# Kernel optimization log

Hardware: AMD Instinct MI355X
Metric: run time of the kernel (lower is better)

Reference implementation:

```python
import jax, jax.numpy as jnp
import numpy as np

N, T, H, W, C = 8, 128, 32, 32, 3
HID = 128
CONV_F = 32
FLAT = H * W * CONV_F  # 32768


def setup_inputs() -> dict:
    key = jax.random.key(0)
    ks = jax.random.split(key, 8)
    def w(k, shape, fan_in):
        return jax.random.normal(k, shape, jnp.float32) / np.sqrt(fan_in)
    x = jax.random.normal(ks[0], (N, T, H, W, C), jnp.float32)
    done = jax.random.randint(ks[1], (N, T), 0, 2, jnp.int32)
    return {
        "x": x,
        "done": done,
        "conv_w": w(ks[2], (3, 3, C, CONV_F), 3 * 3 * C),
        "conv_b": jnp.zeros((CONV_F,), jnp.float32),
        "early_w": w(ks[3], (FLAT, HID), FLAT),
        "early_b": jnp.zeros((HID,), jnp.float32),
        "lstm_wx": w(ks[4], (HID, 4 * HID), HID),
        "lstm_wh": w(ks[5], (HID, 4 * HID), HID),
        "lstm_b": jnp.zeros((4 * HID,), jnp.float32),
        "out_w": w(ks[6], (HID, HID), HID),
        "out_b": jnp.zeros((HID,), jnp.float32),
    }


def _forward(x, done, conv_w, conv_b, early_w, early_b,
             lstm_wx, lstm_wh, lstm_b, out_w, out_b):
    n, t = x.shape[0], x.shape[1]
    # conv encoder over flattened (N*T) frames, SAME padding (flax nn.Conv default)
    xf = x.reshape(n * t, H, W, C)
    xf = jax.lax.conv_general_dilated(
        xf, conv_w, window_strides=(1, 1), padding="SAME",
        dimension_numbers=("NHWC", "HWIO", "NHWC")) + conv_b
    feat = xf.reshape(n, t, -1)  # [N, T, FLAT]
    # early MLP
    feat = jax.nn.relu(feat @ early_w + early_b)  # [N, T, HID]
    # reset-masked LSTM scan over time
    # pre-compute input gate projections for all steps (batched matmul)
    zx = feat @ lstm_wx + lstm_b  # [N, T, 4H]
    zx_t = jnp.swapaxes(zx, 0, 1)       # [T, N, 4H]
    done_t = jnp.swapaxes(done, 0, 1)   # [T, N]

    def step(carry, inp):
        c, h = carry
        zxt, dt = inp
        mask = (dt != 0)[:, None]
        c = jnp.where(mask, 0.0, c)
        h = jnp.where(mask, 0.0, h)
        z = zxt + h @ lstm_wh  # [N, 4H]
        i, f, g, o = jnp.split(z, 4, axis=-1)
        i = jax.nn.sigmoid(i)
        f = jax.nn.sigmoid(f)
        g = jnp.tanh(g)
        o = jax.nn.sigmoid(o)
        c = f * c + i * g
        h = o * jnp.tanh(c)
        return (c, h), h

    init = (jnp.zeros((n, HID), jnp.float32), jnp.zeros((n, HID), jnp.float32))
    (c_fin, h_fin), hs = jax.lax.scan(step, init, (zx_t, done_t))
    hs = jnp.swapaxes(hs, 0, 1)  # [N, T, HID]
    # output MLP
    y = jax.nn.relu(hs @ out_w + out_b)
    return c_fin, h_fin, y


def reference(x, done, conv_w, conv_b, early_w, early_b,
              lstm_wx, lstm_wh, lstm_b, out_w, out_b):
    return _forward(x, done, conv_w, conv_b, early_w, early_b,
                    lstm_wx, lstm_wh, lstm_b, out_w, out_b)
```

## Files before the change

kernel.cpp:

```cpp
#include <hip/hip_runtime.h>


typedef unsigned short ushort_t;
typedef short bf16x8 __attribute__((ext_vector_type(8)));
typedef float f32x4 __attribute__((ext_vector_type(4)));
typedef _Float16 h2 __attribute__((ext_vector_type(2)));

__device__ __forceinline__ ushort_t f2b(float f) {
  unsigned int u = __float_as_uint(f);
  unsigned int r = (u + 0x7fffu + ((u >> 16) & 1u)) >> 16;
  return (ushort_t)r;
}
__device__ __forceinline__ unsigned pack_h2(float a, float b) {
  union { _Float16 h[2]; unsigned u; } v;
  v.h[0] = (_Float16)a; v.h[1] = (_Float16)b; return v.u;
}

#define NT   1024
#define KIN  3072
#define KS   8

__global__ __launch_bounds__(256) void prep_kernel(
    const float* __restrict__ wx, const float* __restrict__ wh,
    const float* __restrict__ ow, const float* __restrict__ eb,
    ushort_t* __restrict__ wxT, unsigned* __restrict__ whT16,
    ushort_t* __restrict__ owT, float* __restrict__ bias2)
{
  const int total = 65536 + 32768 + 16384 + 128;
  for (int i = blockIdx.x * blockDim.x + threadIdx.x; i < total;
       i += gridDim.x * blockDim.x) {
    int j = i;
    if (j < 65536) { int n = j >> 7, k = j & 127; wxT[j] = f2b(wx[k * 512 + n]); continue; }
    j -= 65536;
    if (j < 32768) {
      int col = j >> 6, k2 = j & 63;
      whT16[j] = pack_h2(wh[(2 * k2) * 512 + col], wh[(2 * k2 + 1) * 512 + col]);
      continue;
    }
    j -= 32768;
    if (j < 16384) { int n = j >> 7, k = j & 127; owT[j] = f2b(ow[k * 128 + n]); continue; }
    j -= 16384;
    bias2[j] = eb[j];
  }
}

__global__ __launch_bounds__(128) void build_u(
    const float* __restrict__ conv_w, const float* __restrict__ conv_b,
    const float* __restrict__ early_w,
    ushort_t* __restrict__ UT, float* __restrict__ bias2)
{
  __shared__ float cw[864];
  const int tid = threadIdx.x;
  const int p = blockIdx.x;
  for (int i = tid; i < 864; i += 128) cw[i] = conv_w[i];
  __syncthreads();
  const int hp = p >> 5, wp = p & 31;
  float a0 = 0.f, a1 = 0.f, a2 = 0.f;
  for (int kh = 0; kh < 3; kh++) {
    int h = hp - kh + 1; if ((unsigned)h >= 32u) continue;
    for (int kw = 0; kw < 3; kw++) {
      int w = wp - kw + 1; if ((unsigned)w >= 32u) continue;
      const float* wr = early_w + ((size_t)((h * 32 + w) * 32)) * 128 + tid;
      const float* cwp = cw + (kh * 3 + kw) * 96;
      #pragma unroll 8
      for (int f = 0; f < 32; f++) {
        float wv = wr[f * 128];
        a0 += cwp[f]      * wv;
        a1 += cwp[32 + f] * wv;
        a2 += cwp[64 + f] * wv;
      }
    }
  }
  size_t ub = (size_t)tid * KIN + p * 3;
  UT[ub + 0] = f2b(a0); UT[ub + 1] = f2b(a1); UT[ub + 2] = f2b(a2);

  float cbs = 0.f;
  #pragma unroll 8
  for (int f = 0; f < 32; f++) cbs += __builtin_fabsf(conv_b[f]);
  if (cbs != 0.f && p < 32) {
    float part = 0.f;
    for (int pp = p * 32; pp < p * 32 + 32; pp++)
      for (int f = 0; f < 32; f++)
        part += conv_b[f] * early_w[(size_t)(pp * 32 + f) * 128 + tid];
    atomicAdd(&bias2[tid], part);
  }
}

__global__ __launch_bounds__(256) void feat_gemm(
    const float* __restrict__ x, const ushort_t* __restrict__ UT,
    float* __restrict__ partial)
{
  __shared__ short As[16 * 72];
  __shared__ short Bs[128 * 72];
  const int tid = threadIdx.x;
  const int m0 = blockIdx.x * 16;
  const int ks = blockIdx.y;
  const int wave = tid >> 6, lane = tid & 63;
  const int quad = lane >> 4, l15 = lane & 15;
  const int c0 = wave * 32;

  f32x4 acc0 = {0.f, 0.f, 0.f, 0.f};
  f32x4 acc1 = {0.f, 0.f, 0.f, 0.f};

  const int kend = ks * 384 + 384;
  for (int k0 = ks * 384; k0 < kend; k0 += 64) {
    __syncthreads();
    for (int s = tid; s < 1152; s += 256) {
      if (s < 128) {
        int row = s >> 3, t8 = s & 7;
        const float4* g = (const float4*)(x + (size_t)(m0 + row) * KIN + k0 + t8 * 8);
        float4 f0 = g[0], f1 = g[1];
        ushort_t tmp[8] = {f2b(f0.x), f2b(f0.y), f2b(f0.z), f2b(f0.w),
                           f2b(f1.x), f2b(f1.y), f2b(f1.z), f2b(f1.w)};
        *(uint4*)&As[row * 72 + t8 * 8] = *(const uint4*)tmp;
      } else {
        int s2 = s - 128;
        int row = s2 >> 3, t8 = s2 & 7;
        const uint4* g = (const uint4*)(UT + (size_t)row * KIN + k0 + t8 * 8);
        *(uint4*)&Bs[row * 72 + t8 * 8] = *g;
      }
    }
    __syncthreads();
    #pragma unroll
    for (int kk = 0; kk < 2; kk++) {
      int ko = kk * 32 + quad * 8;
      bf16x8 a  = *(const bf16x8*)&As[l15 * 72 + ko];
      bf16x8 b0 = *(const bf16x8*)&Bs[(c0 + l15) * 72 + ko];
      bf16x8 b1 = *(const bf16x8*)&Bs[(c0 + 16 + l15) * 72 + ko];
      acc0 = __builtin_amdgcn_mfma_f32_16x16x32_bf16(a, b0, acc0, 0, 0, 0);
      acc1 = __builtin_amdgcn_mfma_f32_16x16x32_bf16(a, b1, acc1, 0, 0, 0);
    }
  }
  #pragma unroll
  for (int r = 0; r < 4; r++) {
    int m = m0 + quad * 4 + r;
    size_t base = ((size_t)ks * 1024 + m) * 128;
    partial[base + c0 + l15]      = acc0[r];
    partial[base + c0 + 16 + l15] = acc1[r];
  }
}

__global__ __launch_bounds__(256) void reduce_feat(
    const float* __restrict__ partial, const float* __restrict__ bias2,
    ushort_t* __restrict__ featb)
{
  int i = blockIdx.x * 256 + threadIdx.x;
  float s = bias2[i & 127];
  #pragma unroll
  for (int ks = 0; ks < KS; ks++) s += partial[(size_t)ks * 131072 + i];
  featb[i] = f2b(fmaxf(s, 0.f));
}

__global__ __launch_bounds__(128) void gemm_k128(
    const ushort_t* __restrict__ A, const ushort_t* __restrict__ BT,
    const float* __restrict__ bias,
    float* __restrict__ outf, ushort_t* __restrict__ outb,
    int N, int relu)
{
  __shared__ short As[16 * 136];
  __shared__ short Bs[64 * 136];
  const int tid = threadIdx.x;
  const int m0 = blockIdx.x * 16;
  const int n0 = blockIdx.y * 64;
  const int wave = tid >> 6, lane = tid & 63;
  const int quad = lane >> 4, l15 = lane & 15;
  const int c0 = wave * 32;

  for (int s = tid; s < 1280; s += 128) {
    int row = s >> 4, t8 = s & 15;
    if (s < 256) {
      const uint4* g = (const uint4*)(A + (size_t)(m0 + row) * 128 + t8 * 8);
      *(uint4*)&As[row * 136 + t8 * 8] = *g;
    } else {
      int r2 = row - 16;
      const uint4* g = (const uint4*)(BT + (size_t)(n0 + r2) * 128 + t8 * 8);
      *(uint4*)&Bs[r2 * 136 + t8 * 8] = *g;
    }
  }
  __syncthreads();

  f32x4 acc0 = {0.f, 0.f, 0.f, 0.f};
  f32x4 acc1 = {0.f, 0.f, 0.f, 0.f};
  #pragma unroll
  for (int kk = 0; kk < 4; kk++) {
    int ko = kk * 32 + quad * 8;
    bf16x8 a  = *(const bf16x8*)&As[l15 * 136 + ko];
    bf16x8 b0 = *(const bf16x8*)&Bs[(c0 + l15) * 136 + ko];
    bf16x8 b1 = *(const bf16x8*)&Bs[(c0 + 16 + l15) * 136 + ko];
    acc0 = __builtin_amdgcn_mfma_f32_16x16x32_bf16(a, b0, acc0, 0, 0, 0);
    acc1 = __builtin_amdgcn_mfma_f32_16x16x32_bf16(a, b1, acc1, 0, 0, 0);
  }
  #pragma unroll
  for (int r = 0; r < 4; r++) {
    int m = m0 + quad * 4 + r;
    int n1 = n0 + c0 + l15, n2 = n1 + 16;
    float v1 = acc0[r] + bias[n1];
    float v2 = acc1[r] + bias[n2];
    if (relu) { v1 = fmaxf(v1, 0.f); v2 = fmaxf(v2, 0.f); }
    size_t o1 = (size_t)m * N + n1, o2 = (size_t)m * N + n2;
    if (outf) { outf[o1] = v1; outf[o2] = v2; }
    if (outb) { outb[o1] = f2b(v1); outb[o2] = f2b(v2); }
  }
}

__device__ __forceinline__ float fsig(float x) {
  return 1.f / (1.f + exp2f(-1.44269504f * x));
}
__device__ __forceinline__ float ftanh(float x) {
  float e = exp2f(2.885390082f * x);
  return 1.f - 2.f / (e + 1.f);
}
__device__ __forceinline__ int nth_bit(unsigned long long m0, unsigned long long m1, int i) {
  int c0 = __popcll(m0);
  if (i < c0) {
    unsigned long long m = m0;
    for (int k = 0; k < i; k++) m &= m - 1;
    return __ffsll((long long)m) - 1;
  }
  i -= c0;
  unsigned long long m = m1;
  for (int k = 0; k < i; k++) m &= m - 1;
  return 64 + __ffsll((long long)m) - 1;
}

__global__ __launch_bounds__(512, 2) void lstm_scan(
    const int* __restrict__ done, const float* __restrict__ zx,
    const unsigned* __restrict__ whT16, ushort_t* __restrict__ hsb,
    float* __restrict__ dout)
{
  __shared__ float z_s[512];
  __shared__ _Float16 h16_s[128];
  __shared__ float c_s[128];
  __shared__ unsigned long long masks[16];
  const int tid = threadIdx.x;

  uint4 w4[16];
  {
    const uint4* wp = (const uint4*)(whT16 + (size_t)tid * 64);
    #pragma unroll
    for (int i = 0; i < 16; i++) w4[i] = wp[i];
  }
  const h2* wv = (const h2*)w4;

  for (int n = 0; n < 8; n++) {
    bool flag = false;
    if (tid < 128) flag = (tid == 0) || (done[n * 128 + tid] != 0);
    unsigned long long m = __ballot(flag);
    if (tid == 0)  masks[2*n]     = m;
    if (tid == 64) masks[2*n + 1] = m;
  }
  __syncthreads();

  int total = 0;
  #pragma unroll
  for (int n = 0; n < 8; n++)
    total += __popcll(masks[2*n]) + __popcll(masks[2*n+1]);

  for (int g = blockIdx.x; g < total; g += gridDim.x) {
    int i = g, n = 0, cn = 0;
    for (; n < 8; n++) {
      cn = __popcll(masks[2*n]) + __popcll(masks[2*n+1]);
      if (i < cn) break;
      i -= cn;
    }
    int t0 = nth_bit(masks[2*n], masks[2*n+1], i);
    int t1 = (i + 1 < cn) ? nth_bit(masks[2*n], masks[2*n+1], i + 1) : 128;

    if (tid < 128) { ((ushort_t*)h16_s)[tid] = 0; c_s[tid] = 0.f; }
    __syncthreads();

    float zval = zx[((size_t)n * 128 + t0) * 512 + tid];
    for (int t = t0; t < t1; t++) {
      float znext = 0.f;
      if (t + 1 < t1) znext = zx[((size_t)n * 128 + t + 1) * 512 + tid];
      float a0 = 0.f, a1 = 0.f, a2 = 0.f, a3 = 0.f;
      const float4* hp = (const float4*)h16_s;
      #pragma unroll
      for (int q = 0; q < 16; q++) {
        float4 hb = hp[q];
        const h2* hh = (const h2*)&hb;
        a0 = __builtin_amdgcn_fdot2(wv[4*q+0], hh[0], a0, false);
        a1 = __builtin_amdgcn_fdot2(wv[4*q+1], hh[1], a1, false);
        a2 = __builtin_amdgcn_fdot2(wv[4*q+2], hh[2], a2, false);
        a3 = __builtin_amdgcn_fdot2(wv[4*q+3], hh[3], a3, false);
      }
      z_s[tid] = zval + (a0 + a1) + (a2 + a3);
      __syncthreads();
      if (tid < 128) {
        float ig = fsig(z_s[tid]);
        float fg = fsig(z_s[tid + 128]);
        float gg = ftanh(z_s[tid + 256]);
        float og = fsig(z_s[tid + 384]);
        float c = fg * c_s[tid] + ig * gg;
        float hn = og * ftanh(c);
        c_s[tid] = c;
        h16_s[tid] = (_Float16)hn;
        hsb[((size_t)n * 128 + t) * 128 + tid] = f2b(hn);
        if (t == 127) {
          dout[n * 128 + tid] = c;
          dout[1024 + n * 128 + tid] = hn;
        }
      }
      __syncthreads();
      zval = znext;
    }
  }
}

extern "C" void kernel_launch(void* const* d_in, const int* in_sizes, int n_in,
                              void* d_out, int out_size, void* d_ws, size_t ws_size,
                              hipStream_t stream) {
  const float* x       = (const float*)d_in[0];
  const int*   done    = (const int*)  d_in[1];
  const float* conv_w  = (const float*)d_in[2];
  const float* conv_b  = (const float*)d_in[3];
  const float* early_w = (const float*)d_in[4];
  const float* early_b = (const float*)d_in[5];
  const float* lstm_wx = (const float*)d_in[6];
  const float* lstm_wh = (const float*)d_in[7];
  const float* lstm_b  = (const float*)d_in[8];
  const float* out_w   = (const float*)d_in[9];
  const float* out_b   = (const float*)d_in[10];
  float* dout = (float*)d_out;

  char* ws = (char*)d_ws;
  float*    partial = (float*)   (ws + 0);
  ushort_t* UT      = (ushort_t*)(ws + 4194304);
  ushort_t* featb   = (ushort_t*)(ws + 4980736);
  float*    zx      = (float*)   (ws + 5242880);
  ushort_t* wxT     = (ushort_t*)(ws + 7340032);
  unsigned* whT16   = (unsigned*)(ws + 7471104);
  ushort_t* owT     = (ushort_t*)(ws + 7733248);
  ushort_t* hsb     = (ushort_t*)(ws + 7766016);
  float*    bias2   = (float*)   (ws + 8028160);

  prep_kernel<<<120, 256, 0, stream>>>(lstm_wx, lstm_wh, out_w, early_b,
                                       wxT, whT16, owT, bias2);
  build_u<<<1024, 128, 0, stream>>>(conv_w, conv_b, early_w, UT, bias2);
  feat_gemm<<<dim3(64, KS), 256, 0, stream>>>(x, UT, partial);
  reduce_feat<<<512, 256, 0, stream>>>(partial, bias2, featb);
  gemm_k128<<<dim3(64, 8), 128, 0, stream>>>(featb, wxT, lstm_b, zx, nullptr, 512, 0);
  lstm_scan<<<512, 512, 0, stream>>>(done, zx, whT16, hsb, dout);
  gemm_k128<<<dim3(64, 2), 128, 0, stream>>>(hsb, owT, out_b, dout + 2048, nullptr, 128, 1);
}
```

Before: 154.6 us.

## Fuse all stages into one persistent kernel with global atomic barriers

Replaces the seven launches with one persistent 512-block kernel. Stages are separated by an atomic-counter grid barrier, and the counter is reset by a memset before each launch. The feature-reduce step is folded into the zx GEMM, the feature GEMM gets double-buffered, XOR-swizzled LDS staging, and the LSTM scan uses 256 threads that each handle two gate columns. The goal is to remove launch gaps and the featb round trip. In exchange it relies on all 512 blocks being co-resident for the barrier to avoid deadlock, and it holds more registers per thread in the scan.

```diff
diff --git a/kernel.cpp b/kernel.cpp
--- a/kernel.cpp
+++ b/kernel.cpp
@@ -6,203 +6,16 @@
 typedef float f32x4 __attribute__((ext_vector_type(4)));
 typedef _Float16 h2 __attribute__((ext_vector_type(2)));
 
+#define GRID 512
+
 __device__ __forceinline__ ushort_t f2b(float f) {
-  unsigned int u = __float_as_uint(f);
-  unsigned int r = (u + 0x7fffu + ((u >> 16) & 1u)) >> 16;
-  return (ushort_t)r;
+  unsigned u = __float_as_uint(f);
+  return (ushort_t)((u + 0x7fffu + ((u >> 16) & 1u)) >> 16);
 }
 __device__ __forceinline__ unsigned pack_h2(float a, float b) {
   union { _Float16 h[2]; unsigned u; } v;
   v.h[0] = (_Float16)a; v.h[1] = (_Float16)b; return v.u;
 }
-
-#define NT   1024
-#define KIN  3072
-#define KS   8
-
-__global__ __launch_bounds__(256) void prep_kernel(
-    const float* __restrict__ wx, const float* __restrict__ wh,
-    const float* __restrict__ ow, const float* __restrict__ eb,
-    ushort_t* __restrict__ wxT, unsigned* __restrict__ whT16,
-    ushort_t* __restrict__ owT, float* __restrict__ bias2)
-{
-  const int total = 65536 + 32768 + 16384 + 128;
-  for (int i = blockIdx.x * blockDim.x + threadIdx.x; i < total;
-       i += gridDim.x * blockDim.x) {
-    int j = i;
-    if (j < 65536) { int n = j >> 7, k = j & 127; wxT[j] = f2b(wx[k * 512 + n]); continue; }
-    j -= 65536;
-    if (j < 32768) {
-      int col = j >> 6, k2 = j & 63;
-      whT16[j] = pack_h2(wh[(2 * k2) * 512 + col], wh[(2 * k2 + 1) * 512 + col]);
-      continue;
-    }
-    j -= 32768;
-    if (j < 16384) { int n = j >> 7, k = j & 127; owT[j] = f2b(ow[k * 128 + n]); continue; }
-    j -= 16384;
-    bias2[j] = eb[j];
-  }
-}
-
-__global__ __launch_bounds__(128) void build_u(
-    const float* __restrict__ conv_w, const float* __restrict__ conv_b,
-    const float* __restrict__ early_w,
-    ushort_t* __restrict__ UT, float* __restrict__ bias2)
-{
-  __shared__ float cw[864];
-  const int tid = threadIdx.x;
-  const int p = blockIdx.x;
-  for (int i = tid; i < 864; i += 128) cw[i] = conv_w[i];
-  __syncthreads();
-  const int hp = p >> 5, wp = p & 31;
-  float a0 = 0.f, a1 = 0.f, a2 = 0.f;
-  for (int kh = 0; kh < 3; kh++) {
-    int h = hp - kh + 1; if ((unsigned)h >= 32u) continue;
-    for (int kw = 0; kw < 3; kw++) {
-      int w = wp - kw + 1; if ((unsigned)w >= 32u) continue;
-      const float* wr = early_w + ((size_t)((h * 32 + w) * 32)) * 128 + tid;
-      const float* cwp = cw + (kh * 3 + kw) * 96;
-      #pragma unroll 8
-      for (int f = 0; f < 32; f++) {
-        float wv = wr[f * 128];
-        a0 += cwp[f]      * wv;
-        a1 += cwp[32 + f] * wv;
-        a2 += cwp[64 + f] * wv;
-      }
-    }
-  }
-  size_t ub = (size_t)tid * KIN + p * 3;
-  UT[ub + 0] = f2b(a0); UT[ub + 1] = f2b(a1); UT[ub + 2] = f2b(a2);
-
-  float cbs = 0.f;
-  #pragma unroll 8
-  for (int f = 0; f < 32; f++) cbs += __builtin_fabsf(conv_b[f]);
-  if (cbs != 0.f && p < 32) {
-    float part = 0.f;
-    for (int pp = p * 32; pp < p * 32 + 32; pp++)
-      for (int f = 0; f < 32; f++)
-        part += conv_b[f] * early_w[(size_t)(pp * 32 + f) * 128 + tid];
-    atomicAdd(&bias2[tid], part);
-  }
-}
-
-__global__ __launch_bounds__(256) void feat_gemm(
-    const float* __restrict__ x, const ushort_t* __restrict__ UT,
-    float* __restrict__ partial)
-{
-  __shared__ short As[16 * 72];
-  __shared__ short Bs[128 * 72];
-  const int tid = threadIdx.x;
-  const int m0 = blockIdx.x * 16;
-  const int ks = blockIdx.y;
-  const int wave = tid >> 6, lane = tid & 63;
-  const int quad = lane >> 4, l15 = lane & 15;
-  const int c0 = wave * 32;
-
-  f32x4 acc0 = {0.f, 0.f, 0.f, 0.f};
-  f32x4 acc1 = {0.f, 0.f, 0.f, 0.f};
-
-  const int kend = ks * 384 + 384;
-  for (int k0 = ks * 384; k0 < kend; k0 += 64) {
-    __syncthreads();
-    for (int s = tid; s < 1152; s += 256) {
-      if (s < 128) {
-        int row = s >> 3, t8 = s & 7;
-        const float4* g = (const float4*)(x + (size_t)(m0 + row) * KIN + k0 + t8 * 8);
-        float4 f0 = g[0], f1 = g[1];
-        ushort_t tmp[8] = {f2b(f0.x), f2b(f0.y), f2b(f0.z), f2b(f0.w),
-                           f2b(f1.x), f2b(f1.y), f2b(f1.z), f2b(f1.w)};
-        *(uint4*)&As[row * 72 + t8 * 8] = *(const uint4*)tmp;
-      } else {
-        int s2 = s - 128;
-        int row = s2 >> 3, t8 = s2 & 7;
-        const uint4* g = (const uint4*)(UT + (size_t)row * KIN + k0 + t8 * 8);
-        *(uint4*)&Bs[row * 72 + t8 * 8] = *g;
-      }
-    }
-    __syncthreads();
-    #pragma unroll
-    for (int kk = 0; kk < 2; kk++) {
-      int ko = kk * 32 + quad * 8;
-      bf16x8 a  = *(const bf16x8*)&As[l15 * 72 + ko];
-      bf16x8 b0 = *(const bf16x8*)&Bs[(c0 + l15) * 72 + ko];
-      bf16x8 b1 = *(const bf16x8*)&Bs[(c0 + 16 + l15) * 72 + ko];
-      acc0 = __builtin_amdgcn_mfma_f32_16x16x32_bf16(a, b0, acc0, 0, 0, 0);
-      acc1 = __builtin_amdgcn_mfma_f32_16x16x32_bf16(a, b1, acc1, 0, 0, 0);
-    }
-  }
-  #pragma unroll
-  for (int r = 0; r < 4; r++) {
-    int m = m0 + quad * 4 + r;
-    size_t base = ((size_t)ks * 1024 + m) * 128;
-    partial[base + c0 + l15]      = acc0[r];
-    partial[base + c0 + 16 + l15] = acc1[r];
-  }
-}
-
-__global__ __launch_bounds__(256) void reduce_feat(
-    const float* __restrict__ partial, const float* __restrict__ bias2,
-    ushort_t* __restrict__ featb)
-{
-  int i = blockIdx.x * 256 + threadIdx.x;
-  float s = bias2[i & 127];
-  #pragma unroll
-  for (int ks = 0; ks < KS; ks++) s += partial[(size_t)ks * 131072 + i];
-  featb[i] = f2b(fmaxf(s, 0.f));
-}
-
-__global__ __launch_bounds__(128) void gemm_k128(
-    const ushort_t* __restrict__ A, const ushort_t* __restrict__ BT,
-    const float* __restrict__ bias,
-    float* __restrict__ outf, ushort_t* __restrict__ outb,
-    int N, int relu)
-{
-  __shared__ short As[16 * 136];
-  __shared__ short Bs[64 * 136];
-  const int tid = threadIdx.x;
-  const int m0 = blockIdx.x * 16;
-  const int n0 = blockIdx.y * 64;
-  const int wave = tid >> 6, lane = tid & 63;
-  const int quad = lane >> 4, l15 = lane & 15;
-  const int c0 = wave * 32;
-
-  for (int s = tid; s < 1280; s += 128) {
-    int row = s >> 4, t8 = s & 15;
-    if (s < 256) {
-      const uint4* g = (const uint4*)(A + (size_t)(m0 + row) * 128 + t8 * 8);
-      *(uint4*)&As[row * 136 + t8 * 8] = *g;
-    } else {
-      int r2 = row - 16;
-      const uint4* g = (const uint4*)(BT + (size_t)(n0 + r2) * 128 + t8 * 8);
-      *(uint4*)&Bs[r2 * 136 + t8 * 8] = *g;
-    }
-  }
-  __syncthreads();
-
-  f32x4 acc0 = {0.f, 0.f, 0.f, 0.f};
-  f32x4 acc1 = {0.f, 0.f, 0.f, 0.f};
-  #pragma unroll
-  for (int kk = 0; kk < 4; kk++) {
-    int ko = kk * 32 + quad * 8;
-    bf16x8 a  = *(const bf16x8*)&As[l15 * 136 + ko];
-    bf16x8 b0 = *(const bf16x8*)&Bs[(c0 + l15) * 136 + ko];
-    bf16x8 b1 = *(const bf16x8*)&Bs[(c0 + 16 + l15) * 136 + ko];
-    acc0 = __builtin_amdgcn_mfma_f32_16x16x32_bf16(a, b0, acc0, 0, 0, 0);
-    acc1 = __builtin_amdgcn_mfma_f32_16x16x32_bf16(a, b1, acc1, 0, 0, 0);
-  }
-  #pragma unroll
-  for (int r = 0; r < 4; r++) {
-    int m = m0 + quad * 4 + r;
-    int n1 = n0 + c0 + l15, n2 = n1 + 16;
-    float v1 = acc0[r] + bias[n1];
-    float v2 = acc1[r] + bias[n2];
-    if (relu) { v1 = fmaxf(v1, 0.f); v2 = fmaxf(v2, 0.f); }
-    size_t o1 = (size_t)m * N + n1, o2 = (size_t)m * N + n2;
-    if (outf) { outf[o1] = v1; outf[o2] = v2; }
-    if (outb) { outb[o1] = f2b(v1); outb[o2] = f2b(v2); }
-  }
-}
-
 __device__ __forceinline__ float fsig(float x) {
   return 1.f / (1.f + exp2f(-1.44269504f * x));
 }
@@ -223,86 +36,319 @@
   return 64 + __ffsll((long long)m) - 1;
 }
 
-__global__ __launch_bounds__(512, 2) void lstm_scan(
-    const int* __restrict__ done, const float* __restrict__ zx,
-    const unsigned* __restrict__ whT16, ushort_t* __restrict__ hsb,
-    float* __restrict__ dout)
+__device__ __forceinline__ void gbar(unsigned* ctr, unsigned target) {
+  __syncthreads();
+  if (threadIdx.x == 0) {
+    __hip_atomic_fetch_add(ctr, 1u, __ATOMIC_RELEASE, __HIP_MEMORY_SCOPE_AGENT);
+    while (__hip_atomic_load(ctr, __ATOMIC_ACQUIRE, __HIP_MEMORY_SCOPE_AGENT) < target)
+      __builtin_amdgcn_s_sleep(8);
+  }
+  __syncthreads();
+}
+
+__global__ __launch_bounds__(256, 2) void mega(
+    const float* __restrict__ x, const int* __restrict__ done,
+    const float* __restrict__ conv_w, const float* __restrict__ conv_b,
+    const float* __restrict__ early_w, const float* __restrict__ eb,
+    const float* __restrict__ wx, const float* __restrict__ wh,
+    const float* __restrict__ lstm_b, const float* __restrict__ ow,
+    const float* __restrict__ out_b,
+    unsigned* __restrict__ ctr, float* __restrict__ partial,
+    ushort_t* __restrict__ UT, float* __restrict__ zx,
+    ushort_t* __restrict__ wxT, unsigned* __restrict__ whT16,
+    ushort_t* __restrict__ owT, ushort_t* __restrict__ hsb,
+    float* __restrict__ bias2, float* __restrict__ dout)
 {
-  __shared__ float z_s[512];
-  __shared__ _Float16 h16_s[128];
-  __shared__ float c_s[128];
-  __shared__ unsigned long long masks[16];
+  __shared__ union {
+    float cw[864];
+    short ft[2][9216];
+    short g2[18432];
+    struct { float z[512]; float c[128]; _Float16 h16[128];
+             unsigned long long masks[16]; } ls;
+  } L;
+
   const int tid = threadIdx.x;
-
-  uint4 w4[16];
+  const int b = blockIdx.x;
+  const int wave = tid >> 6, lane = tid & 63;
+  const int quad = lane >> 4, l15 = lane & 15;
+  const int c0 = wave * 32;
+
   {
-    const uint4* wp = (const uint4*)(whT16 + (size_t)tid * 64);
-    #pragma unroll
-    for (int i = 0; i < 16; i++) w4[i] = wp[i];
-  }
-  const h2* wv = (const h2*)w4;
-
-  for (int n = 0; n < 8; n++) {
-    bool flag = false;
-    if (tid < 128) flag = (tid == 0) || (done[n * 128 + tid] != 0);
-    unsigned long long m = __ballot(flag);
-    if (tid == 0)  masks[2*n]     = m;
-    if (tid == 64) masks[2*n + 1] = m;
-  }
-  __syncthreads();
-
-  int total = 0;
-  #pragma unroll
-  for (int n = 0; n < 8; n++)
-    total += __popcll(masks[2*n]) + __popcll(masks[2*n+1]);
-
-  for (int g = blockIdx.x; g < total; g += gridDim.x) {
-    int i = g, n = 0, cn = 0;
-    for (; n < 8; n++) {
-      cn = __popcll(masks[2*n]) + __popcll(masks[2*n+1]);
-      if (i < cn) break;
-      i -= cn;
-    }
-    int t0 = nth_bit(masks[2*n], masks[2*n+1], i);
-    int t1 = (i + 1 < cn) ? nth_bit(masks[2*n], masks[2*n+1], i + 1) : 128;
-
-    if (tid < 128) { ((ushort_t*)h16_s)[tid] = 0; c_s[tid] = 0.f; }
+    int i = b * 256 + tid;
+    if (i < 65536) { int n = i >> 7, k = i & 127; wxT[i] = f2b(wx[k * 512 + n]); }
+    else if (i < 98304) { int j = i - 65536; int col = j >> 6, k2 = j & 63;
+      whT16[j] = pack_h2(wh[(2 * k2) * 512 + col], wh[(2 * k2 + 1) * 512 + col]); }
+    else if (i < 114688) { int j = i - 98304; int n = j >> 7, k = j & 127;
+      owT[j] = f2b(ow[k * 128 + n]); }
+    else if (i < 114816) { bias2[i - 114688] = eb[i - 114688]; }
+
+    for (int q = tid; q < 864; q += 256) L.cw[q] = conv_w[q];
     __syncthreads();
-
-    float zval = zx[((size_t)n * 128 + t0) * 512 + tid];
-    for (int t = t0; t < t1; t++) {
-      float znext = 0.f;
-      if (t + 1 < t1) znext = zx[((size_t)n * 128 + t + 1) * 512 + tid];
-      float a0 = 0.f, a1 = 0.f, a2 = 0.f, a3 = 0.f;
-      const float4* hp = (const float4*)h16_s;
-      #pragma unroll
-      for (int q = 0; q < 16; q++) {
-        float4 hb = hp[q];
-        const h2* hh = (const h2*)&hb;
-        a0 = __builtin_amdgcn_fdot2(wv[4*q+0], hh[0], a0, false);
-        a1 = __builtin_amdgcn_fdot2(wv[4*q+1], hh[1], a1, false);
-        a2 = __builtin_amdgcn_fdot2(wv[4*q+2], hh[2], a2, false);
-        a3 = __builtin_amdgcn_fdot2(wv[4*q+3], hh[3], a3, false);
-      }
-      z_s[tid] = zval + (a0 + a1) + (a2 + a3);
+    const int o = tid & 127, grp = tid >> 7;
+    const int px = (b & 7) * 128 + ((b >> 3) << 1) + grp;
+    const int hp = px >> 5, wp = px & 31;
+    float a0 = 0.f, a1 = 0.f, a2 = 0.f;
+    for (int kh = 0; kh < 3; kh++) {
+      int h = hp - kh + 1; if ((unsigned)h >= 32u) continue;
+      for (int kw = 0; kw < 3; kw++) {
+        int w = wp - kw + 1; if ((unsigned)w >= 32u) continue;
+        const float* wr = early_w + ((size_t)((h * 32 + w) * 32)) * 128 + o;
+        const float* cwp = L.cw + (kh * 3 + kw) * 96;
+        #pragma unroll 8
+        for (int f = 0; f < 32; f++) {
+          float wv = wr[f * 128];
+          a0 += cwp[f]      * wv;
+          a1 += cwp[32 + f] * wv;
+          a2 += cwp[64 + f] * wv;
+        }
+      }
+    }
+    size_t ub = (size_t)o * 3072 + px * 3;
+    UT[ub + 0] = f2b(a0); UT[ub + 1] = f2b(a1); UT[ub + 2] = f2b(a2);
+
+    float cbs = 0.f;
+    #pragma unroll 8
+    for (int f = 0; f < 32; f++) cbs += __builtin_fabsf(conv_b[f]);
+    if (cbs != 0.f && px < 32) {
+      float part = 0.f;
+      for (int pp = px * 32; pp < px * 32 + 32; pp++)
+        for (int f = 0; f < 32; f++)
+          part += conv_b[f] * early_w[(size_t)(pp * 32 + f) * 128 + o];
+      atomicAdd(&bias2[o], part);
+    }
+  }
+  gbar(ctr, GRID);
+
+  {
+    const int m0 = (b & 63) * 16;
+    const int ks = b >> 6;
+    const int kb = ks * 384;
+    const bool isA = tid < 128;
+    const int arow = tid >> 3, ag = tid & 7;
+    const int s2base = tid ^ 128;
+
+    float4 fa0, fa1; uint4 rb[4];
+    f32x4 acc0 = {0.f, 0.f, 0.f, 0.f};
+    f32x4 acc1 = {0.f, 0.f, 0.f, 0.f};
+
+    auto load = [&](int k0) {
+      if (isA) {
+        const float4* p = (const float4*)(x + (size_t)(m0 + arow) * 3072 + k0 + ag * 8);
+        fa0 = p[0]; fa1 = p[1];
+      }
+      #pragma unroll
+      for (int j = 0; j < 4; j++) {
+        int s2 = s2base + 256 * j, row = s2 >> 3, g = s2 & 7;
+        rb[j] = *(const uint4*)(UT + (size_t)row * 3072 + k0 + g * 8);
+      }
+    };
+    auto stage = [&](int p) {
+      #pragma unroll
+      for (int j = 0; j < 4; j++) {
+        int s2 = s2base + 256 * j, row = s2 >> 3, g = s2 & 7;
+        *(uint4*)&L.ft[p][1024 + row * 64 + (((g ^ row) & 7) * 8)] = rb[j];
+      }
+      if (isA) {
+        union { ushort_t us[8]; uint4 v; } t8;
+        t8.us[0] = f2b(fa0.x); t8.us[1] = f2b(fa0.y); t8.us[2] = f2b(fa0.z); t8.us[3] = f2b(fa0.w);
+        t8.us[4] = f2b(fa1.x); t8.us[5] = f2b(fa1.y); t8.us[6] = f2b(fa1.z); t8.us[7] = f2b(fa1.w);
+        *(uint4*)&L.ft[p][arow * 64 + (((ag ^ arow) & 7) * 8)] = t8.v;
+      }
+    };
+
+    load(kb);
+    for (int it = 0; it < 6; it++) {
+      const int p = it & 1;
+      stage(p);
       __syncthreads();
-      if (tid < 128) {
-        float ig = fsig(z_s[tid]);
-        float fg = fsig(z_s[tid + 128]);
-        float gg = ftanh(z_s[tid + 256]);
-        float og = fsig(z_s[tid + 384]);
-        float c = fg * c_s[tid] + ig * gg;
-        float hn = og * ftanh(c);
-        c_s[tid] = c;
-        h16_s[tid] = (_Float16)hn;
-        hsb[((size_t)n * 128 + t) * 128 + tid] = f2b(hn);
-        if (t == 127) {
-          dout[n * 128 + tid] = c;
-          dout[1024 + n * 128 + tid] = hn;
+      if (it < 5) load(kb + (it + 1) * 64);
+      const short* As = &L.ft[p][0];
+      const short* Bs = &L.ft[p][1024];
+      #pragma unroll
+      for (int kk = 0; kk < 2; kk++) {
+        int gp = kk * 4 + quad;
+        bf16x8 a  = *(const bf16x8*)&As[l15 * 64 + (((gp ^ l15) & 7) * 8)];
+        bf16x8 b0 = *(const bf16x8*)&Bs[(c0 + l15) * 64 + (((gp ^ (c0 + l15)) & 7) * 8)];
+        bf16x8 b1 = *(const bf16x8*)&Bs[(c0 + 16 + l15) * 64 + (((gp ^ (c0 + l15)) & 7) * 8)];
+        acc0 = __builtin_amdgcn_mfma_f32_16x16x32_bf16(a, b0, acc0, 0, 0, 0);
+        acc1 = __builtin_amdgcn_mfma_f32_16x16x32_bf16(a, b1, acc1, 0, 0, 0);
+      }
+    }
+    #pragma unroll
+    for (int r = 0; r < 4; r++) {
+      int m = m0 + quad * 4 + r;
+      size_t base = ((size_t)ks * 1024 + m) * 128;
+      partial[base + c0 + l15]      = acc0[r];
+      partial[base + c0 + 16 + l15] = acc1[r];
+    }
+  }
+  gbar(ctr, 2 * GRID);
+
+  if (b < 256) {
+    const int m0 = (b & 63) * 16;
+    const int n0 = (b >> 6) * 128;
+    {
+      int r = tid >> 4, gA = tid & 15, cb = gA * 8;
+      float4 s0 = {0,0,0,0}, s1 = {0,0,0,0};
+      #pragma unroll
+      for (int ks = 0; ks < 8; ks++) {
+        const float4* p = (const float4*)(partial + (size_t)ks * 131072 + (m0 + r) * 128 + cb);
+        float4 u0 = p[0], u1 = p[1];
+        s0.x += u0.x; s0.y += u0.y; s0.z += u0.z; s0.w += u0.w;
+        s1.x += u1.x; s1.y += u1.y; s1.z += u1.z; s1.w += u1.w;
+      }
+      const float* bp = bias2 + cb;
+      union { ushort_t us[8]; uint4 v; } t8;
+      t8.us[0] = f2b(fmaxf(s0.x + bp[0], 0.f)); t8.us[1] = f2b(fmaxf(s0.y + bp[1], 0.f));
+      t8.us[2] = f2b(fmaxf(s0.z + bp[2], 0.f)); t8.us[3] = f2b(fmaxf(s0.w + bp[3], 0.f));
+      t8.us[4] = f2b(fmaxf(s1.x + bp[4], 0.f)); t8.us[5] = f2b(fmaxf(s1.y + bp[5], 0.f));
+      t8.us[6] = f2b(fmaxf(s1.z + bp[6], 0.f)); t8.us[7] = f2b(fmaxf(s1.w + bp[7], 0.f));
+      *(uint4*)&L.g2[r * 128 + (((gA ^ r) & 15) * 8)] = t8.v;
+    }
+    #pragma unroll
+    for (int j = 0; j < 8; j++) {
+      int s = tid + 256 * j, row = s >> 4, g = s & 15;
+      uint4 v = *(const uint4*)(wxT + (size_t)(n0 + row) * 128 + g * 8);
+      *(uint4*)&L.g2[2048 + row * 128 + (((g ^ row) & 15) * 8)] = v;
+    }
+    __syncthreads();
+    f32x4 acc0 = {0,0,0,0}, acc1 = {0,0,0,0};
+    #pragma unroll
+    for (int kk = 0; kk < 4; kk++) {
+      int gp = kk * 4 + quad;
+      bf16x8 a  = *(const bf16x8*)&L.g2[l15 * 128 + (((gp ^ l15) & 15) * 8)];
+      bf16x8 b0 = *(const bf16x8*)&L.g2[2048 + (c0 + l15) * 128 + (((gp ^ l15) & 15) * 8)];
+      bf16x8 b1 = *(const bf16x8*)&L.g2[2048 + (c0 + 16 + l15) * 128 + (((gp ^ l15) & 15) * 8)];
+      acc0 = __builtin_amdgcn_mfma_f32_16x16x32_bf16(a, b0, acc0, 0, 0, 0);
+      acc1 = __builtin_amdgcn_mfma_f32_16x16x32_bf16(a, b1, acc1, 0, 0, 0);
+    }
+    #pragma unroll
+    for (int r = 0; r < 4; r++) {
+      int m = m0 + quad * 4 + r;
+      int n1 = n0 + c0 + l15, n2 = n1 + 16;
+      zx[(size_t)m * 512 + n1] = acc0[r] + lstm_b[n1];
+      zx[(size_t)m * 512 + n2] = acc1[r] + lstm_b[n2];
+    }
+  }
+  gbar(ctr, 3 * GRID);
+
+  {
+    uint4 w1[16], w2[16];
+    {
+      const uint4* p1 = (const uint4*)(whT16 + (size_t)tid * 64);
+      const uint4* p2 = (const uint4*)(whT16 + (size_t)(tid + 256) * 64);
+      #pragma unroll
+      for (int i = 0; i < 16; i++) { w1[i] = p1[i]; w2[i] = p2[i]; }
+    }
+    const h2* wa = (const h2*)w1;
+    const h2* wb = (const h2*)w2;
+
+    for (int n = 0; n < 8; n++) {
+      bool flag = false;
+      if (tid < 128) flag = (tid == 0) || (done[n * 128 + tid] != 0);
+      unsigned long long m = __ballot(flag);
+      if (tid == 0)  L.ls.masks[2 * n]     = m;
+      if (tid == 64) L.ls.masks[2 * n + 1] = m;
+    }
+    __syncthreads();
+
+    int total = 0;
+    #pragma unroll
+    for (int n = 0; n < 8; n++)
+      total += __popcll(L.ls.masks[2 * n]) + __popcll(L.ls.masks[2 * n + 1]);
+
+    for (int g = b; g < total; g += GRID) {
+      int i = g, n = 0, cn = 0;
+      for (; n < 8; n++) {
+        cn = __popcll(L.ls.masks[2 * n]) + __popcll(L.ls.masks[2 * n + 1]);
+        if (i < cn) break;
+        i -= cn;
+      }
+      int t0 = nth_bit(L.ls.masks[2 * n], L.ls.masks[2 * n + 1], i);
+      int t1 = (i + 1 < cn) ? nth_bit(L.ls.masks[2 * n], L.ls.masks[2 * n + 1], i + 1) : 128;
+
+      if (tid < 128) { ((ushort_t*)L.ls.h16)[tid] = 0; L.ls.c[tid] = 0.f; }
+      __syncthreads();
+
+      float z1 = zx[((size_t)n * 128 + t0) * 512 + tid];
+      float z2 = zx[((size_t)n * 128 + t0) * 512 + tid + 256];
+      for (int t = t0; t < t1; t++) {
+        float z1n = 0.f, z2n = 0.f;
+        if (t + 1 < t1) {
+          z1n = zx[((size_t)n * 128 + t + 1) * 512 + tid];
+          z2n = zx[((size_t)n * 128 + t + 1) * 512 + tid + 256];
         }
-      }
-      __syncthreads();
-      zval = znext;
+        float a0 = 0.f, a1 = 0.f, a2 = 0.f, a3 = 0.f;
+        float b0 = 0.f, b1 = 0.f, b2 = 0.f, b3 = 0.f;
+        const float4* hp = (const float4*)L.ls.h16;
+        #pragma unroll
+        for (int q = 0; q < 16; q++) {
+          float4 hb = hp[q];
+          const h2* hh = (const h2*)&hb;
+          a0 = __builtin_amdgcn_fdot2(wa[4*q+0], hh[0], a0, false);
+          a1 = __builtin_amdgcn_fdot2(wa[4*q+1], hh[1], a1, false);
+          a2 = __builtin_amdgcn_fdot2(wa[4*q+2], hh[2], a2, false);
+          a3 = __builtin_amdgcn_fdot2(wa[4*q+3], hh[3], a3, false);
+          b0 = __builtin_amdgcn_fdot2(wb[4*q+0], hh[0], b0, false);
+          b1 = __builtin_amdgcn_fdot2(wb[4*q+1], hh[1], b1, false);
+          b2 = __builtin_amdgcn_fdot2(wb[4*q+2], hh[2], b2, false);
+          b3 = __builtin_amdgcn_fdot2(wb[4*q+3], hh[3], b3, false);
+        }
+        L.ls.z[tid]       = z1 + (a0 + a1) + (a2 + a3);
+        L.ls.z[tid + 256] = z2 + (b0 + b1) + (b2 + b3);
+        __syncthreads();
+        if (tid < 128) {
+          float ig = fsig(L.ls.z[tid]);
+          float fg = fsig(L.ls.z[tid + 128]);
+          float gg = ftanh(L.ls.z[tid + 256]);
+          float og = fsig(L.ls.z[tid + 384]);
+          float c = fg * L.ls.c[tid] + ig * gg;
+          float hn = og * ftanh(c);
+          L.ls.c[tid] = c;
+          L.ls.h16[tid] = (_Float16)hn;
+          hsb[((size_t)n * 128 + t) * 128 + tid] = f2b(hn);
+          if (t == 127) {
+            dout[n * 128 + tid] = c;
+            dout[1024 + n * 128 + tid] = hn;
+          }
+        }
+        __syncthreads();
+        z1 = z1n; z2 = z2n;
+      }
+    }
+  }
+  gbar(ctr, 4 * GRID);
+
+  if (b < 64) {
+    const int m0 = b * 16;
+    {
+      int r = tid >> 4, g = tid & 15;
+      uint4 av = *(const uint4*)(hsb + (size_t)(m0 + r) * 128 + g * 8);
+      *(uint4*)&L.g2[r * 128 + (((g ^ r) & 15) * 8)] = av;
+    }
+    #pragma unroll
+    for (int j = 0; j < 8; j++) {
+      int s = tid + 256 * j, row = s >> 4, g = s & 15;
+      uint4 v = *(const uint4*)(owT + (size_t)row * 128 + g * 8);
+      *(uint4*)&L.g2[2048 + row * 128 + (((g ^ row) & 15) * 8)] = v;
+    }
+    __syncthreads();
+    f32x4 acc0 = {0,0,0,0}, acc1 = {0,0,0,0};
+    #pragma unroll
+    for (int kk = 0; kk < 4; kk++) {
+      int gp = kk * 4 + quad;
+      bf16x8 a  = *(const bf16x8*)&L.g2[l15 * 128 + (((gp ^ l15) & 15) * 8)];
+      bf16x8 b0 = *(const bf16x8*)&L.g2[2048 + (c0 + l15) * 128 + (((gp ^ l15) & 15) * 8)];
+      bf16x8 b1 = *(const bf16x8*)&L.g2[2048 + (c0 + 16 + l15) * 128 + (((gp ^ l15) & 15) * 8)];
+      acc0 = __builtin_amdgcn_mfma_f32_16x16x32_bf16(a, b0, acc0, 0, 0, 0);
+      acc1 = __builtin_amdgcn_mfma_f32_16x16x32_bf16(a, b1, acc1, 0, 0, 0);
+    }
+    #pragma unroll
+    for (int r = 0; r < 4; r++) {
+      int m = m0 + quad * 4 + r;
+      int n1 = c0 + l15, n2 = n1 + 16;
+      dout[2048 + (size_t)m * 128 + n1] = fmaxf(acc0[r] + out_b[n1], 0.f);
+      dout[2048 + (size_t)m * 128 + n2] = fmaxf(acc1[r] + out_b[n2], 0.f);
     }
   }
 }
@@ -324,22 +370,19 @@
   float* dout = (float*)d_out;
 
   char* ws = (char*)d_ws;
-  float*    partial = (float*)   (ws + 0);
-  ushort_t* UT      = (ushort_t*)(ws + 4194304);
-  ushort_t* featb   = (ushort_t*)(ws + 4980736);
-  float*    zx      = (float*)   (ws + 5242880);
-  ushort_t* wxT     = (ushort_t*)(ws + 7340032);
-  unsigned* whT16   = (unsigned*)(ws + 7471104);
-  ushort_t* owT     = (ushort_t*)(ws + 7733248);
-  ushort_t* hsb     = (ushort_t*)(ws + 7766016);
-  float*    bias2   = (float*)   (ws + 8028160);
-
-  prep_kernel<<<120, 256, 0, stream>>>(lstm_wx, lstm_wh, out_w, early_b,
-                                       wxT, whT16, owT, bias2);
-  build_u<<<1024, 128, 0, stream>>>(conv_w, conv_b, early_w, UT, bias2);
-  feat_gemm<<<dim3(64, KS), 256, 0, stream>>>(x, UT, partial);
-  reduce_feat<<<512, 256, 0, stream>>>(partial, bias2, featb);
-  gemm_k128<<<dim3(64, 8), 128, 0, stream>>>(featb, wxT, lstm_b, zx, nullptr, 512, 0);
-  lstm_scan<<<512, 512, 0, stream>>>(done, zx, whT16, hsb, dout);
-  gemm_k128<<<dim3(64, 2), 128, 0, stream>>>(hsb, owT, out_b, dout + 2048, nullptr, 128, 1);
-}
+  unsigned* ctrp    = (unsigned*)(ws + 0);
+  float*    partial = (float*)   (ws + 4096);
+  ushort_t* UT      = (ushort_t*)(ws + 4198400);
+  float*    zx      = (float*)   (ws + 4984832);
+  ushort_t* wxT     = (ushort_t*)(ws + 7081984);
+  unsigned* whT16   = (unsigned*)(ws + 7213056);
+  ushort_t* owT     = (ushort_t*)(ws + 7344128);
+  ushort_t* hsb     = (ushort_t*)(ws + 7376896);
+  float*    bias2   = (float*)   (ws + 7639040);
+
+  hipMemsetAsync(ctrp, 0, 256, stream);
+  mega<<<GRID, 256, 0, stream>>>(x, done, conv_w, conv_b, early_w, early_b,
+                                 lstm_wx, lstm_wh, lstm_b, out_w, out_b,
+                                 ctrp, partial, UT, zx, wxT, whT16, owT, hsb,
+                                 bias2, dout);
+}
```

Measured after the change: 374.9 us. 142% more time.

## Fuse pipeline kernels: merge prep into build, reduce into zx GEMM, output MLP into scan

Applied to the files above, without the earlier changes.

Merges the weight prep kernel and the conv-folded weight builder into one launch. Folds the split-K reduction and ReLU into the zx GEMM, which now uses 128-wide N tiles. Moves the output MLP into the LSTM scan as per-step fp16 dot products, which removes the hs buffer and one GEMM launch. In exchange the scan adds serial work inside each step and drops the zx prefetch, and the fp16 output weights may cost accuracy.

```diff
diff --git a/kernel.cpp b/kernel.cpp
--- a/kernel.cpp
+++ b/kernel.cpp
@@ -7,51 +7,63 @@
 typedef _Float16 h2 __attribute__((ext_vector_type(2)));
 
 __device__ __forceinline__ ushort_t f2b(float f) {
-  unsigned int u = __float_as_uint(f);
-  unsigned int r = (u + 0x7fffu + ((u >> 16) & 1u)) >> 16;
-  return (ushort_t)r;
+  unsigned u = __float_as_uint(f);
+  return (ushort_t)((u + 0x7fffu + ((u >> 16) & 1u)) >> 16);
 }
 __device__ __forceinline__ unsigned pack_h2(float a, float b) {
   union { _Float16 h[2]; unsigned u; } v;
   v.h[0] = (_Float16)a; v.h[1] = (_Float16)b; return v.u;
 }
-
-#define NT   1024
-#define KIN  3072
-#define KS   8
-
-__global__ __launch_bounds__(256) void prep_kernel(
+__device__ __forceinline__ float fsig(float x) {
+  return 1.f / (1.f + exp2f(-1.44269504f * x));
+}
+__device__ __forceinline__ float ftanh(float x) {
+  float e = exp2f(2.885390082f * x);
+  return 1.f - 2.f / (e + 1.f);
+}
+__device__ __forceinline__ int nth_bit(unsigned long long m0, unsigned long long m1, int i) {
+  int c0 = __popcll(m0);
+  if (i < c0) {
+    unsigned long long m = m0;
+    for (int k = 0; k < i; k++) m &= m - 1;
+    return __ffsll((long long)m) - 1;
+  }
+  i -= c0;
+  unsigned long long m = m1;
+  for (int k = 0; k < i; k++) m &= m - 1;
+  return 64 + __ffsll((long long)m) - 1;
+}
+
+__global__ __launch_bounds__(128) void prep_build(
+    const float* __restrict__ conv_w, const float* __restrict__ conv_b,
+    const float* __restrict__ early_w, const float* __restrict__ eb,
     const float* __restrict__ wx, const float* __restrict__ wh,
-    const float* __restrict__ ow, const float* __restrict__ eb,
-    ushort_t* __restrict__ wxT, unsigned* __restrict__ whT16,
-    ushort_t* __restrict__ owT, float* __restrict__ bias2)
+    const float* __restrict__ ow,
+    ushort_t* __restrict__ UT, ushort_t* __restrict__ wxT,
+    unsigned* __restrict__ whT16, unsigned* __restrict__ owT16,
+    float* __restrict__ bias2)
 {
-  const int total = 65536 + 32768 + 16384 + 128;
-  for (int i = blockIdx.x * blockDim.x + threadIdx.x; i < total;
-       i += gridDim.x * blockDim.x) {
-    int j = i;
-    if (j < 65536) { int n = j >> 7, k = j & 127; wxT[j] = f2b(wx[k * 512 + n]); continue; }
-    j -= 65536;
-    if (j < 32768) {
-      int col = j >> 6, k2 = j & 63;
-      whT16[j] = pack_h2(wh[(2 * k2) * 512 + col], wh[(2 * k2 + 1) * 512 + col]);
-      continue;
-    }
-    j -= 32768;
-    if (j < 16384) { int n = j >> 7, k = j & 127; owT[j] = f2b(ow[k * 128 + n]); continue; }
-    j -= 16384;
-    bias2[j] = eb[j];
-  }
-}
-
-__global__ __launch_bounds__(128) void build_u(
-    const float* __restrict__ conv_w, const float* __restrict__ conv_b,
-    const float* __restrict__ early_w,
-    ushort_t* __restrict__ UT, float* __restrict__ bias2)
-{
+  const int tid = threadIdx.x;
+  const int b = blockIdx.x;
+
+  if (b >= 1024) {
+    for (int i = (b - 1024) * 128 + tid; i < 131200; i += 128 * 128) {
+      int j = i;
+      if (j < 65536) { int n = j >> 7, k = j & 127; wxT[j] = f2b(wx[k * 512 + n]); continue; }
+      j -= 65536;
+      if (j < 32768) { int col = j >> 6, k2 = j & 63;
+        whT16[j] = pack_h2(wh[(2 * k2) * 512 + col], wh[(2 * k2 + 1) * 512 + col]); continue; }
+      j -= 32768;
+      if (j < 32768) { int col = j >> 6, k2 = j & 63;
+        owT16[j] = pack_h2(ow[(2 * k2) * 128 + col], ow[(2 * k2 + 1) * 128 + col]); continue; }
+      j -= 32768;
+      bias2[j] = eb[j];
+    }
+    return;
+  }
+
   __shared__ float cw[864];
-  const int tid = threadIdx.x;
-  const int p = blockIdx.x;
+  const int p = b;
   for (int i = tid; i < 864; i += 128) cw[i] = conv_w[i];
   __syncthreads();
   const int hp = p >> 5, wp = p & 31;
@@ -71,7 +83,7 @@
       }
     }
   }
-  size_t ub = (size_t)tid * KIN + p * 3;
+  size_t ub = (size_t)tid * 3072 + p * 3;
   UT[ub + 0] = f2b(a0); UT[ub + 1] = f2b(a1); UT[ub + 2] = f2b(a2);
 
   float cbs = 0.f;
@@ -108,7 +120,7 @@
     for (int s = tid; s < 1152; s += 256) {
       if (s < 128) {
         int row = s >> 3, t8 = s & 7;
-        const float4* g = (const float4*)(x + (size_t)(m0 + row) * KIN + k0 + t8 * 8);
+        const float4* g = (const float4*)(x + (size_t)(m0 + row) * 3072 + k0 + t8 * 8);
         float4 f0 = g[0], f1 = g[1];
         ushort_t tmp[8] = {f2b(f0.x), f2b(f0.y), f2b(f0.z), f2b(f0.w),
                            f2b(f1.x), f2b(f1.y), f2b(f1.z), f2b(f1.w)};
@@ -116,7 +128,7 @@
       } else {
         int s2 = s - 128;
         int row = s2 >> 3, t8 = s2 & 7;
-        const uint4* g = (const uint4*)(UT + (size_t)row * KIN + k0 + t8 * 8);
+        const uint4* g = (const uint4*)(UT + (size_t)row * 3072 + k0 + t8 * 8);
         *(uint4*)&Bs[row * 72 + t8 * 8] = *g;
       }
     }
@@ -140,47 +152,47 @@
   }
 }
 
-__global__ __launch_bounds__(256) void reduce_feat(
+__global__ __launch_bounds__(256) void zx_gemm(
     const float* __restrict__ partial, const float* __restrict__ bias2,
-    ushort_t* __restrict__ featb)
-{
-  int i = blockIdx.x * 256 + threadIdx.x;
-  float s = bias2[i & 127];
-  #pragma unroll
-  for (int ks = 0; ks < KS; ks++) s += partial[(size_t)ks * 131072 + i];
-  featb[i] = f2b(fmaxf(s, 0.f));
-}
-
-__global__ __launch_bounds__(128) void gemm_k128(
-    const ushort_t* __restrict__ A, const ushort_t* __restrict__ BT,
-    const float* __restrict__ bias,
-    float* __restrict__ outf, ushort_t* __restrict__ outb,
-    int N, int relu)
+    const ushort_t* __restrict__ wxT, const float* __restrict__ lstm_b,
+    float* __restrict__ zx)
 {
   __shared__ short As[16 * 136];
-  __shared__ short Bs[64 * 136];
+  __shared__ short Bs[128 * 136];
   const int tid = threadIdx.x;
   const int m0 = blockIdx.x * 16;
-  const int n0 = blockIdx.y * 64;
+  const int n0 = blockIdx.y * 128;
   const int wave = tid >> 6, lane = tid & 63;
   const int quad = lane >> 4, l15 = lane & 15;
   const int c0 = wave * 32;
 
-  for (int s = tid; s < 1280; s += 128) {
-    int row = s >> 4, t8 = s & 15;
-    if (s < 256) {
-      const uint4* g = (const uint4*)(A + (size_t)(m0 + row) * 128 + t8 * 8);
-      *(uint4*)&As[row * 136 + t8 * 8] = *g;
-    } else {
-      int r2 = row - 16;
-      const uint4* g = (const uint4*)(BT + (size_t)(n0 + r2) * 128 + t8 * 8);
-      *(uint4*)&Bs[r2 * 136 + t8 * 8] = *g;
-    }
+  {
+    int r = tid >> 4, gA = tid & 15, cb = gA * 8;
+    float4 s0 = {0,0,0,0}, s1 = {0,0,0,0};
+    #pragma unroll
+    for (int ks = 0; ks < 8; ks++) {
+      const float4* p = (const float4*)(partial + (size_t)ks * 131072 + (m0 + r) * 128 + cb);
+      float4 u0 = p[0], u1 = p[1];
+      s0.x += u0.x; s0.y += u0.y; s0.z += u0.z; s0.w += u0.w;
+      s1.x += u1.x; s1.y += u1.y; s1.z += u1.z; s1.w += u1.w;
+    }
+    const float* bp = bias2 + cb;
+    union { ushort_t us[8]; uint4 v; } t8;
+    t8.us[0] = f2b(fmaxf(s0.x + bp[0], 0.f)); t8.us[1] = f2b(fmaxf(s0.y + bp[1], 0.f));
+    t8.us[2] = f2b(fmaxf(s0.z + bp[2], 0.f)); t8.us[3] = f2b(fmaxf(s0.w + bp[3], 0.f));
+    t8.us[4] = f2b(fmaxf(s1.x + bp[4], 0.f)); t8.us[5] = f2b(fmaxf(s1.y + bp[5], 0.f));
+    t8.us[6] = f2b(fmaxf(s1.z + bp[6], 0.f)); t8.us[7] = f2b(fmaxf(s1.w + bp[7], 0.f));
+    *(uint4*)&As[r * 136 + gA * 8] = t8.v;
+  }
+  #pragma unroll
+  for (int j = 0; j < 8; j++) {
+    int s = tid + 256 * j, row = s >> 4, g = s & 15;
+    uint4 v = *(const uint4*)(wxT + (size_t)(n0 + row) * 128 + g * 8);
+    *(uint4*)&Bs[row * 136 + g * 8] = v;
   }
   __syncthreads();
 
-  f32x4 acc0 = {0.f, 0.f, 0.f, 0.f};
-  f32x4 acc1 = {0.f, 0.f, 0.f, 0.f};
+  f32x4 acc0 = {0,0,0,0}, acc1 = {0,0,0,0};
   #pragma unroll
   for (int kk = 0; kk < 4; kk++) {
     int ko = kk * 32 + quad * 8;
@@ -194,43 +206,19 @@
   for (int r = 0; r < 4; r++) {
     int m = m0 + quad * 4 + r;
     int n1 = n0 + c0 + l15, n2 = n1 + 16;
-    float v1 = acc0[r] + bias[n1];
-    float v2 = acc1[r] + bias[n2];
-    if (relu) { v1 = fmaxf(v1, 0.f); v2 = fmaxf(v2, 0.f); }
-    size_t o1 = (size_t)m * N + n1, o2 = (size_t)m * N + n2;
-    if (outf) { outf[o1] = v1; outf[o2] = v2; }
-    if (outb) { outb[o1] = f2b(v1); outb[o2] = f2b(v2); }
-  }
-}
-
-__device__ __forceinline__ float fsig(float x) {
-  return 1.f / (1.f + exp2f(-1.44269504f * x));
-}
-__device__ __forceinline__ float ftanh(float x) {
-  float e = exp2f(2.885390082f * x);
-  return 1.f - 2.f / (e + 1.f);
-}
-__device__ __forceinline__ int nth_bit(unsigned long long m0, unsigned long long m1, int i) {
-  int c0 = __popcll(m0);
-  if (i < c0) {
-    unsigned long long m = m0;
-    for (int k = 0; k < i; k++) m &= m - 1;
-    return __ffsll((long long)m) - 1;
-  }
-  i -= c0;
-  unsigned long long m = m1;
-  for (int k = 0; k < i; k++) m &= m - 1;
-  return 64 + __ffsll((long long)m) - 1;
-}
-
-__global__ __launch_bounds__(512, 2) void lstm_scan(
+    zx[(size_t)m * 512 + n1] = acc0[r] + lstm_b[n1];
+    zx[(size_t)m * 512 + n2] = acc1[r] + lstm_b[n2];
+  }
+}
+
+__global__ __launch_bounds__(512, 1) void lstm_scan(
     const int* __restrict__ done, const float* __restrict__ zx,
-    const unsigned* __restrict__ whT16, ushort_t* __restrict__ hsb,
-    float* __restrict__ dout)
+    const unsigned* __restrict__ whT16, const unsigned* __restrict__ owT16,
+    const float* __restrict__ out_b, float* __restrict__ dout)
 {
   __shared__ float z_s[512];
+  __shared__ float c_s[128];
   __shared__ _Float16 h16_s[128];
-  __shared__ float c_s[128];
   __shared__ unsigned long long masks[16];
   const int tid = threadIdx.x;
 
@@ -242,37 +230,44 @@
   }
   const h2* wv = (const h2*)w4;
 
+  uint4 o4[16];
+  if (tid < 128) {
+    const uint4* op = (const uint4*)(owT16 + (size_t)tid * 64);
+    #pragma unroll
+    for (int i = 0; i < 16; i++) o4[i] = op[i];
+  }
+  const h2* ov = (const h2*)o4;
+  const float ob = (tid < 128) ? out_b[tid] : 0.f;
+
   for (int n = 0; n < 8; n++) {
     bool flag = false;
     if (tid < 128) flag = (tid == 0) || (done[n * 128 + tid] != 0);
     unsigned long long m = __ballot(flag);
-    if (tid == 0)  masks[2*n]     = m;
-    if (tid == 64) masks[2*n + 1] = m;
+    if (tid == 0)  masks[2 * n]     = m;
+    if (tid == 64) masks[2 * n + 1] = m;
   }
   __syncthreads();
 
   int total = 0;
   #pragma unroll
   for (int n = 0; n < 8; n++)
-    total += __popcll(masks[2*n]) + __popcll(masks[2*n+1]);
+    total += __popcll(masks[2 * n]) + __popcll(masks[2 * n + 1]);
 
   for (int g = blockIdx.x; g < total; g += gridDim.x) {
     int i = g, n = 0, cn = 0;
     for (; n < 8; n++) {
-      cn = __popcll(masks[2*n]) + __popcll(masks[2*n+1]);
+      cn = __popcll(masks[2 * n]) + __popcll(masks[2 * n + 1]);
       if (i < cn) break;
       i -= cn;
     }
-    int t0 = nth_bit(masks[2*n], masks[2*n+1], i);
-    int t1 = (i + 1 < cn) ? nth_bit(masks[2*n], masks[2*n+1], i + 1) : 128;
+    int t0 = nth_bit(masks[2 * n], masks[2 * n + 1], i);
+    int t1 = (i + 1 < cn) ? nth_bit(masks[2 * n], masks[2 * n + 1], i + 1) : 128;
 
     if (tid < 128) { ((ushort_t*)h16_s)[tid] = 0; c_s[tid] = 0.f; }
     __syncthreads();
 
-    float zval = zx[((size_t)n * 128 + t0) * 512 + tid];
     for (int t = t0; t < t1; t++) {
-      float znext = 0.f;
-      if (t + 1 < t1) znext = zx[((size_t)n * 128 + t + 1) * 512 + tid];
+      float zval = zx[((size_t)n * 128 + t) * 512 + tid];
       float a0 = 0.f, a1 = 0.f, a2 = 0.f, a3 = 0.f;
       const float4* hp = (const float4*)h16_s;
       #pragma unroll
@@ -295,14 +290,27 @@
         float hn = og * ftanh(c);
         c_s[tid] = c;
         h16_s[tid] = (_Float16)hn;
-        hsb[((size_t)n * 128 + t) * 128 + tid] = f2b(hn);
         if (t == 127) {
           dout[n * 128 + tid] = c;
           dout[1024 + n * 128 + tid] = hn;
         }
       }
       __syncthreads();
-      zval = znext;
+      if (tid < 128) {
+        float y0 = 0.f, y1 = 0.f, y2 = 0.f, y3 = 0.f;
+        const float4* hq = (const float4*)h16_s;
+        #pragma unroll
+        for (int q = 0; q < 16; q++) {
+          float4 hb = hq[q];
+          const h2* hh = (const h2*)&hb;
+          y0 = __builtin_amdgcn_fdot2(ov[4*q+0], hh[0], y0, false);
+          y1 = __builtin_amdgcn_fdot2(ov[4*q+1], hh[1], y1, false);
+          y2 = __builtin_amdgcn_fdot2(ov[4*q+2], hh[2], y2, false);
+          y3 = __builtin_amdgcn_fdot2(ov[4*q+3], hh[3], y3, false);
+        }
+        dout[2048 + ((size_t)n * 128 + t) * 128 + tid] =
+            fmaxf((y0 + y1) + (y2 + y3) + ob, 0.f);
+      }
     }
   }
 }
@@ -326,20 +334,16 @@
   char* ws = (char*)d_ws;
   float*    partial = (float*)   (ws + 0);
   ushort_t* UT      = (ushort_t*)(ws + 4194304);
-  ushort_t* featb   = (ushort_t*)(ws + 4980736);
-  float*    zx      = (float*)   (ws + 5242880);
-  ushort_t* wxT     = (ushort_t*)(ws + 7340032);
-  unsigned* whT16   = (unsigned*)(ws + 7471104);
-  ushort_t* owT     = (ushort_t*)(ws + 7733248);
-  ushort_t* hsb     = (ushort_t*)(ws + 7766016);
-  float*    bias2   = (float*)   (ws + 8028160);
-
-  prep_kernel<<<120, 256, 0, stream>>>(lstm_wx, lstm_wh, out_w, early_b,
-                                       wxT, whT16, owT, bias2);
-  build_u<<<1024, 128, 0, stream>>>(conv_w, conv_b, early_w, UT, bias2);
-  feat_gemm<<<dim3(64, KS), 256, 0, stream>>>(x, UT, partial);
-  reduce_feat<<<512, 256, 0, stream>>>(partial, bias2, featb);
-  gemm_k128<<<dim3(64, 8), 128, 0, stream>>>(featb, wxT, lstm_b, zx, nullptr, 512, 0);
-  lstm_scan<<<512, 512, 0, stream>>>(done, zx, whT16, hsb, dout);
-  gemm_k128<<<dim3(64, 2), 128, 0, stream>>>(hsb, owT, out_b, dout + 2048, nullptr, 128, 1);
-}
+  float*    zx      = (float*)   (ws + 4980736);
+  ushort_t* wxT     = (ushort_t*)(ws + 7077888);
+  unsigned* whT16   = (unsigned*)(ws + 7208960);
+  unsigned* owT16   = (unsigned*)(ws + 7340032);
+  float*    bias2   = (float*)   (ws + 7471104);
+
+  prep_build<<<1152, 128, 0, stream>>>(conv_w, conv_b, early_w, early_b,
+                                       lstm_wx, lstm_wh, out_w,
+                                       UT, wxT, whT16, owT16, bias2);
+  feat_gemm<<<dim3(64, 8), 256, 0, stream>>>(x, UT, partial);
+  zx_gemm<<<dim3(64, 4), 256, 0, stream>>>(partial, bias2, wxT, lstm_b, zx);
+  lstm_scan<<<512, 512, 0, stream>>>(done, zx, whT16, owT16, out_b, dout);
+}
```

New measurement: 153.7 us. No clear change (-0.5%).
